# Performance work log

Measured on AMD Instinct MI355X. Metric: run time of the kernel, lower is better.

The kernel has to match this reference:

```python
import jax, jax.numpy as jnp
import numpy as np

B, S, D_IN, D_OUT = 4, 2048, 4096, 4096
ALPHA, INSCALE = 0.001, 0.05


def setup_inputs() -> dict:
    key = jax.random.key(0)
    kx, kw = jax.random.split(key)
    x = jax.random.normal(kx, (B, S, D_IN), dtype=jnp.float32)
    # int8 weight in [-127, 126], matching torch.randint(-127, 127, ...)
    weight = jax.random.randint(kw, (D_OUT, D_IN), -127, 127, dtype=jnp.int32).astype(jnp.int8)
    return {
        "x": x,
        "weight": weight,
        "alpha": jnp.float32(ALPHA),
        "inscale": jnp.float32(INSCALE),
    }


def reference(x, weight, alpha, inscale):
    x_shape = x.shape
    xf = x.reshape(-1, x_shape[-1])                        # [M, K]
    # dynamic per-tensor int8 quantization of activations
    q = jnp.clip(jnp.round(xf / inscale), -128, 127).astype(jnp.int8)
    y = jax.lax.dot_general(
        q, weight,
        dimension_numbers=(((1,), (1,)), ((), ())),
        preferred_element_type=jnp.int32,
    )
    # dequant epilogue: scalar alpha scale -> fp32
    y = y.astype(jnp.float32) * alpha
    return y.reshape(*x_shape[:-1], -1)                    # [B, S, N]
```

## Files before the change

kernel.cpp:

```cpp
#include <hip/hip_runtime.h>
#include <cstdint>


typedef int v4i  __attribute__((ext_vector_type(4)));
typedef int v16i __attribute__((ext_vector_type(16)));

#define BM 256
#define BN 256
#define BKB 64
#define LDS_TILE (BM * BKB)
#define LDS_BUF  (2 * LDS_TILE)
#define NBUF 3

__global__ void prep_kernel(const float* __restrict__ x,
                            signed char* __restrict__ q,
                            const int* __restrict__ w32,
                            signed char* __restrict__ w8,
                            const float* __restrict__ inscale_ptr,
                            int nq, int total) {
    const float s = *inscale_ptr;
    const int stride = gridDim.x * blockDim.x;
    for (int i = blockIdx.x * blockDim.x + threadIdx.x; i < total; i += stride) {
        if (i < nq) {
            float4 f = ((const float4*)x)[i];
            union { signed char c[4]; int v; } u;
            float vals[4] = {f.x, f.y, f.z, f.w};
#pragma unroll
            for (int e = 0; e < 4; ++e) {
                float r = rintf(vals[e] / s);
                r = fminf(fmaxf(r, -128.0f), 127.0f);
                u.c[e] = (signed char)(int)r;
            }
            ((int*)q)[i] = u.v;
        } else {
            const int j = i - nq;
            int4 w = ((const int4*)w32)[j];
            union { signed char c[4]; int v; } u;
            u.c[0] = (signed char)w.x;
            u.c[1] = (signed char)w.y;
            u.c[2] = (signed char)w.z;
            u.c[3] = (signed char)w.w;
            ((int*)w8)[j] = u.v;
        }
    }
}

__device__ __forceinline__ void async16(void* lds, const void* g) {
    __builtin_amdgcn_global_load_lds(
        (const __attribute__((address_space(1))) void*)g,
        (__attribute__((address_space(3))) void*)lds,
        16, 0, 0);
}

__global__ __launch_bounds__(512, 2)
void w8a8_gemm(const signed char* __restrict__ A,
               const signed char* __restrict__ Bw,
               float* __restrict__ C,
               const float* __restrict__ alpha_ptr,
               int M, int N, int K) {
    __shared__ signed char lds[NBUF * LDS_BUF];

    const int t    = threadIdx.x;
    const int lane = t & 63;
    const int wave = t >> 6;
    const int wm   = (wave >> 2) * 128;
    const int wn   = (wave & 3) * 64;

    const int nbx   = N / BN;
    const int swz   = ((int)blockIdx.x & 7) * ((int)gridDim.x >> 3)
                    + ((int)blockIdx.x >> 3);
    const int tileM = (swz / nbx) * BM;
    const int tileN = (swz % nbx) * BN;

    const int srow = t >> 2;
    const int sg   = (t & 3) ^ ((t >> 3) & 3);
    const size_t aOff0 = (size_t)(tileM + srow)       * K + sg * 16;
    const size_t aOff1 = (size_t)(tileM + 128 + srow) * K + sg * 16;
    const size_t bOff0 = (size_t)(tileN + srow)       * K + sg * 16;
    const size_t bOff1 = (size_t)(tileN + 128 + srow) * K + sg * 16;
    const int ldst = t * 16;

    auto stageA = [&](int kt, int buf) {
        const size_t ko = (size_t)kt * BKB;
        signed char* d = &lds[buf * LDS_BUF];
        async16(d + ldst,        A + aOff0 + ko);
        async16(d + 8192 + ldst, A + aOff1 + ko);
    };
    auto stageB = [&](int kt, int buf) {
        const size_t ko = (size_t)kt * BKB;
        signed char* d = &lds[buf * LDS_BUF + LDS_TILE];
        async16(d + ldst,        Bw + bOff0 + ko);
        async16(d + 8192 + ldst, Bw + bOff1 + ko);
    };

    const int mrow  = lane & 31;
    const int khalf = lane >> 5;
    const int fswz  = (mrow >> 1) & 3;
    const int offS[2] = { ((0 + khalf) ^ fswz) * 16,
                          ((2 + khalf) ^ fswz) * 16 };
    int arow[4], brow[2];
#pragma unroll
    for (int im = 0; im < 4; ++im) arow[im] = (wm + im * 32 + mrow) * BKB;
#pragma unroll
    for (int jn = 0; jn < 2; ++jn) brow[jn] = LDS_TILE + (wn + jn * 32 + mrow) * BKB;

    v16i acc[4][2] = {};

    stageA(0, 0); stageB(0, 0);
    stageA(1, 1); stageB(1, 1);
    asm volatile("s_waitcnt vmcnt(4)" ::: "memory");
    __builtin_amdgcn_s_barrier();

    const int NT = K / BKB;
    int bc = 0, sb = 2;
#pragma unroll 1
    for (int kt = 0; kt < NT; ++kt) {
        const bool doStage = (kt + 2) < NT;
        const signed char* cb = &lds[bc * LDS_BUF];

        v4i a[2][4], b[2][2];
#pragma unroll
        for (int s = 0; s < 2; ++s) {
            const int offp = offS[s];
#pragma unroll
            for (int im = 0; im < 4; ++im)
                a[s][im] = *(const v4i*)(cb + arow[im] + offp);
#pragma unroll
            for (int jn = 0; jn < 2; ++jn)
                b[s][jn] = *(const v4i*)(cb + brow[jn] + offp);
        }

        if (doStage) { stageA(kt + 2, sb); stageB(kt + 2, sb); }

        __builtin_amdgcn_s_setprio(1);
#pragma unroll
        for (int s = 0; s < 2; ++s)
#pragma unroll
            for (int im = 0; im < 4; ++im)
#pragma unroll
                for (int jn = 0; jn < 2; ++jn)
                    acc[im][jn] = __builtin_amdgcn_mfma_i32_32x32x32_i8(
                        a[s][im], b[s][jn], acc[im][jn], 0, 0, 0);
        __builtin_amdgcn_s_setprio(0);

        if (doStage) asm volatile("s_waitcnt vmcnt(4)" ::: "memory");
        else         asm volatile("s_waitcnt vmcnt(0)" ::: "memory");
        __builtin_amdgcn_s_barrier();

        bc = (bc == NBUF - 1) ? 0 : bc + 1;
        sb = (sb == NBUF - 1) ? 0 : sb + 1;
    }

    const float alpha = *alpha_ptr;
    const int ccol  = lane & 31;
    const int rquad = khalf * 4;
#pragma unroll
    for (int im = 0; im < 4; ++im) {
#pragma unroll
        for (int jn = 0; jn < 2; ++jn) {
            const int baseRow = tileM + wm + im * 32;
            const int col     = tileN + wn + jn * 32 + ccol;
#pragma unroll
            for (int reg = 0; reg < 16; ++reg) {
                const int row = baseRow + (reg & 3) + 8 * (reg >> 2) + rquad;
                C[(size_t)row * N + col] = (float)acc[im][jn][reg] * alpha;
            }
        }
    }
}

extern "C" void kernel_launch(void* const* d_in, const int* in_sizes, int n_in,
                              void* d_out, int out_size, void* d_ws, size_t ws_size,
                              hipStream_t stream) {
    const float* x       = (const float*)d_in[0];
    const int*   w32     = (const int*)d_in[1];
    const float* alpha   = (const float*)d_in[2];
    const float* inscale = (const float*)d_in[3];
    float*       out     = (float*)d_out;

    const int K = 4096;
    const int N = 4096;
    const int M = in_sizes[0] / K;

    signed char* q  = (signed char*)d_ws;
    signed char* w8 = (signed char*)d_ws + (size_t)M * K;

    const int nq    = (M * K) / 4;
    const int total = nq + (N * K) / 4;
    prep_kernel<<<2048, 256, 0, stream>>>(x, q, w32, w8, inscale, nq, total);

    dim3 grid((M / BM) * (N / BN));
    w8a8_gemm<<<grid, 512, 0, stream>>>(q, w8, out, alpha, M, N, K);
}
```

Baseline: 406.3 us.

## Switch GEMM main loop to double-buffered 128-wide K stages with interleaved LDS reads

The triple-buffered pipeline with 64-byte K steps becomes a double-buffered one where each stage loads 128 bytes of K (two 64-wide subtiles each of A and B). The result is half as many barriers and loop iterations. Inside an iteration, LDS reads for later subtiles are interleaved with MFMAs on earlier ones to hide LDS latency. The cost is that each iteration now waits for all outstanding global loads (vmcnt(0)), giving only one stage of prefetch distance, and the larger in-flight fragment arrays add register pressure. LDS usage grows from 96KB to 128KB per block, which could limit the two-blocks-per-CU target.

```diff
diff --git a/kernel.cpp b/kernel.cpp
--- a/kernel.cpp
+++ b/kernel.cpp
@@ -7,10 +7,9 @@
 
 #define BM 256
 #define BN 256
-#define BKB 64
-#define LDS_TILE (BM * BKB)
-#define LDS_BUF  (2 * LDS_TILE)
-#define NBUF 3
+#define SUBT 16384
+#define LDS_BUF (4 * SUBT)
+#define NBUF 2
 
 __global__ void prep_kernel(const float* __restrict__ x,
                             signed char* __restrict__ q,
@@ -80,17 +79,16 @@
     const size_t bOff1 = (size_t)(tileN + 128 + srow) * K + sg * 16;
     const int ldst = t * 16;
 
-    auto stageA = [&](int kt, int buf) {
-        const size_t ko = (size_t)kt * BKB;
-        signed char* d = &lds[buf * LDS_BUF];
-        async16(d + ldst,        A + aOff0 + ko);
-        async16(d + 8192 + ldst, A + aOff1 + ko);
-    };
-    auto stageB = [&](int kt, int buf) {
-        const size_t ko = (size_t)kt * BKB;
-        signed char* d = &lds[buf * LDS_BUF + LDS_TILE];
-        async16(d + ldst,        Bw + bOff0 + ko);
-        async16(d + 8192 + ldst, Bw + bOff1 + ko);
+    auto stagePair = [&](int P, signed char* dst) {
+        const size_t k0 = (size_t)P * 128;
+        async16(dst + 0 * SUBT +        ldst, A  + aOff0 + k0);
+        async16(dst + 0 * SUBT + 8192 + ldst, A  + aOff1 + k0);
+        async16(dst + 1 * SUBT +        ldst, A  + aOff0 + k0 + 64);
+        async16(dst + 1 * SUBT + 8192 + ldst, A  + aOff1 + k0 + 64);
+        async16(dst + 2 * SUBT +        ldst, Bw + bOff0 + k0);
+        async16(dst + 2 * SUBT + 8192 + ldst, Bw + bOff1 + k0);
+        async16(dst + 3 * SUBT +        ldst, Bw + bOff0 + k0 + 64);
+        async16(dst + 3 * SUBT + 8192 + ldst, Bw + bOff1 + k0 + 64);
     };
 
     const int mrow  = lane & 31;
@@ -100,55 +98,58 @@
                           ((2 + khalf) ^ fswz) * 16 };
     int arow[4], brow[2];
 #pragma unroll
-    for (int im = 0; im < 4; ++im) arow[im] = (wm + im * 32 + mrow) * BKB;
+    for (int im = 0; im < 4; ++im) arow[im] = (wm + im * 32 + mrow) * 64;
 #pragma unroll
-    for (int jn = 0; jn < 2; ++jn) brow[jn] = LDS_TILE + (wn + jn * 32 + mrow) * BKB;
+    for (int jn = 0; jn < 2; ++jn) brow[jn] = (wn + jn * 32 + mrow) * 64;
 
     v16i acc[4][2] = {};
 
-    stageA(0, 0); stageB(0, 0);
-    stageA(1, 1); stageB(1, 1);
-    asm volatile("s_waitcnt vmcnt(4)" ::: "memory");
+    v4i a[2][2][4], b[2][2][2];
+
+    auto readSet = [&](const signed char* cb, int t2, int s) {
+        const signed char* ab = cb + t2 * SUBT;
+        const signed char* bb = cb + 2 * SUBT + t2 * SUBT;
+        const int offp = offS[s];
+#pragma unroll
+        for (int im = 0; im < 4; ++im)
+            a[t2][s][im] = *(const v4i*)(ab + arow[im] + offp);
+#pragma unroll
+        for (int jn = 0; jn < 2; ++jn)
+            b[t2][s][jn] = *(const v4i*)(bb + brow[jn] + offp);
+    };
+    auto mfmaSet = [&](int t2, int s) {
+        __builtin_amdgcn_s_setprio(1);
+#pragma unroll
+        for (int im = 0; im < 4; ++im)
+#pragma unroll
+            for (int jn = 0; jn < 2; ++jn)
+                acc[im][jn] = __builtin_amdgcn_mfma_i32_32x32x32_i8(
+                    a[t2][s][im], b[t2][s][jn], acc[im][jn], 0, 0, 0);
+        __builtin_amdgcn_s_setprio(0);
+    };
+
+    stagePair(0, &lds[0]);
+    asm volatile("s_waitcnt vmcnt(0)" ::: "memory");
     __builtin_amdgcn_s_barrier();
 
-    const int NT = K / BKB;
-    int bc = 0, sb = 2;
+    const int NP = K / 128;
 #pragma unroll 1
-    for (int kt = 0; kt < NT; ++kt) {
-        const bool doStage = (kt + 2) < NT;
-        const signed char* cb = &lds[bc * LDS_BUF];
+    for (int P = 0; P < NP; ++P) {
+        const signed char* cb = &lds[(P & 1) * LDS_BUF];
 
-        v4i a[2][4], b[2][2];
-#pragma unroll
-        for (int s = 0; s < 2; ++s) {
-            const int offp = offS[s];
-#pragma unroll
-            for (int im = 0; im < 4; ++im)
-                a[s][im] = *(const v4i*)(cb + arow[im] + offp);
-#pragma unroll
-            for (int jn = 0; jn < 2; ++jn)
-                b[s][jn] = *(const v4i*)(cb + brow[jn] + offp);
-        }
+        if (P + 1 < NP) stagePair(P + 1, &lds[((P + 1) & 1) * LDS_BUF]);
 
-        if (doStage) { stageA(kt + 2, sb); stageB(kt + 2, sb); }
+        readSet(cb, 0, 0);
+        readSet(cb, 0, 1);
+        mfmaSet(0, 0);
+        readSet(cb, 1, 0);
+        mfmaSet(0, 1);
+        readSet(cb, 1, 1);
+        mfmaSet(1, 0);
+        mfmaSet(1, 1);
 
-        __builtin_amdgcn_s_setprio(1);
-#pragma unroll
-        for (int s = 0; s < 2; ++s)
-#pragma unroll
-            for (int im = 0; im < 4; ++im)
-#pragma unroll
-                for (int jn = 0; jn < 2; ++jn)
-                    acc[im][jn] = __builtin_amdgcn_mfma_i32_32x32x32_i8(
-                        a[s][im], b[s][jn], acc[im][jn], 0, 0, 0);
-        __builtin_amdgcn_s_setprio(0);
-
-        if (doStage) asm volatile("s_waitcnt vmcnt(4)" ::: "memory");
-        else         asm volatile("s_waitcnt vmcnt(0)" ::: "memory");
+        asm volatile("s_waitcnt vmcnt(0)" ::: "memory");
         __builtin_amdgcn_s_barrier();
-
-        bc = (bc == NBUF - 1) ? 0 : bc + 1;
-        sb = (sb == NBUF - 1) ? 0 : sb + 1;
     }
 
     const float alpha = *alpha_ptr;
```

New measurement: 415.8 us. 2.3% more time.
